# Kernel tuning notes

Measured on AMD Instinct MI355X. Metric: run time of the kernel, lower is better.

Reference implementation:

```python
import jax, jax.numpy as jnp
import numpy as np

B, IN, OUT, P, NS = 256, 1024, 512, 1000, 128

def setup_inputs() -> dict:
    key = jax.random.key(0)
    ks = jax.random.split(key, 6)
    return {
        "x": jax.random.normal(ks[0], (B, IN), jnp.float32),
        "noise": jax.random.normal(ks[1], (B, NS, P), jnp.float32),
        "fb_w": jax.random.normal(ks[2], (1, IN), jnp.float32) * (1.0 / np.sqrt(IN)),
        "fb_b": jnp.zeros((1,), jnp.float32),
        "decay_param": jnp.full((1,), 0.1, jnp.float32),
        "conv_w": jax.random.normal(ks[3], (P, P, 3), jnp.float32) * (1.0 / np.sqrt(3 * P)),
        "conv_b": jnp.zeros((P,), jnp.float32),
        "out_w": jax.random.normal(ks[4], (OUT, P), jnp.float32) * (1.0 / np.sqrt(P)),
        "out_b": jnp.zeros((OUT,), jnp.float32),
    }


def reference(x, noise, fb_w, fb_b, decay_param, conv_w, conv_b, out_w, out_b):
    # x: [B, IN]; noise: [B, NS, P] (Brownian increments for the SDE kernel)
    n_steps = noise.shape[1]
    dt = 1.0 / n_steps                       # T = 1.0
    sd = jnp.sqrt(jnp.asarray(dt, x.dtype))
    # per-sample feedback value: sigmoid(feedback_controller(x))
    feedback = jax.nn.sigmoid(x @ fb_w.T + fb_b)            # [B, 1]
    # decay value: sigmoid(decay_controller) * 0.5 (scalar)
    decay = jax.nn.sigmoid(decay_param[0]) * 0.5
    retain = 1.0 - decay * dt
    # Batched Euler-Maruyama Brownian SDE: X_{t+1} = (1 - decay*dt) X_t + feedback*sqrt(dt)*eps_t
    eps = jnp.transpose(noise, (1, 0, 2))                    # [NS, B, P]
    x0 = jnp.zeros((x.shape[0], noise.shape[2]), x.dtype)

    def step(X, e):
        Xn = X * retain + feedback * sd * e
        return Xn, Xn

    _, paths = jax.lax.scan(step, x0, eps)                   # [NS, B, P]
    paths_bct = jnp.transpose(paths, (1, 2, 0))              # [B, P, NS]
    # temporal_aggregator: Conv1d(P, P, kernel=3, padding=1) over time, then mean over time
    agg = jax.lax.conv_general_dilated(
        paths_bct, conv_w, window_strides=(1,), padding=[(1, 1)],
        dimension_numbers=("NCH", "OIH", "NCH"))
    agg = (agg + conv_b[None, :, None]).mean(axis=2)         # [B, P]
    # output_projection: P -> OUT
    return agg @ out_w.T + out_b
```

## Files before the change

### kernel.cpp

```cpp
#include <hip/hip_runtime.h>
#include <hip/hip_bf16.h>

#define B_N   256
#define IN_N  1024
#define OUT_N 512
#define P_N   1000
#define NS_N  128

#define K1P   3072
#define N1P   1024
#define K2P   1024
#define SK1   16
#define SK2   8

typedef __attribute__((ext_vector_type(8))) short short8v;
typedef __attribute__((ext_vector_type(4))) float f32x4;
typedef unsigned short ushort_t;

__device__ __forceinline__ float sigmoid_f(float z) { return 1.0f / (1.0f + __expf(-z)); }

__device__ __forceinline__ ushort_t f2bf(float x) {
    return __bfloat16_as_ushort(__float2bfloat16(x));
}

__global__ __launch_bounds__(256) void sde_fused_kernel(const float* __restrict__ x,
                                                        const float* __restrict__ fb_w,
                                                        const float* __restrict__ fb_b,
                                                        const float* __restrict__ noise,
                                                        const float* __restrict__ decay_param,
                                                        ushort_t* __restrict__ Thi) {
    const int b  = blockIdx.x;
    const int ch = blockIdx.y;
    const int t  = threadIdx.x;
    const int cg = t & 127;
    const int th = t >> 7;

    float4 xv = ((const float4*)(x + (size_t)b * IN_N))[t];
    float4 wv = ((const float4*)fb_w)[t];
    float s = xv.x * wv.x + xv.y * wv.y + xv.z * wv.z + xv.w * wv.w;
    __shared__ float red[256];
    red[t] = s;
    __syncthreads();
    for (int off = 128; off >= 1; off >>= 1) {
        if (t < off) red[t] += red[t + off];
        __syncthreads();
    }
    float fbv = sigmoid_f(red[0] + fb_b[0]);

    float decay = sigmoid_f(decay_param[0]) * 0.5f;
    const float dt = 1.0f / NS_N;
    float retain = 1.0f - decay * dt;
    float inv_omr = 1.0f / (decay * dt);
    float r2 = retain * retain, r4 = r2 * r2, r8 = r4 * r4;
    float r16 = r8 * r8, r32 = r16 * r16, r64 = r32 * r32;

    const int c0 = ch * 512 + cg * 4;
    const bool act = (c0 < P_N);

    float4 sE = {0, 0, 0, 0}, L = {0, 0, 0, 0}, F = {0, 0, 0, 0};
    if (act) {
        const float* base = noise + (size_t)b * NS_N * P_N + c0;
        const int s0 = th * 64;
        float rp = 1.0f;
        #pragma unroll 16
        for (int ss = s0 + 63; ss >= s0; --ss) {
            float4 e = *(const float4*)(base + (size_t)ss * P_N);
            sE.x += e.x; sE.y += e.y; sE.z += e.z; sE.w += e.w;
            L.x += rp * e.x; L.y += rp * e.y; L.z += rp * e.z; L.w += rp * e.w;
            if (ss == 0) F = e;
            rp *= retain;
        }
    }

    __shared__ float4 xSE[128], xL[128], xF[128];
    if (th == 0) { xSE[cg] = sE; xL[cg] = L; xF[cg] = F; }
    __syncthreads();

    if (th == 1) {
        size_t tb = (size_t)b * K1P + 3 * (size_t)c0;
        if (!act) {
            #pragma unroll
            for (int j = 0; j < 12; ++j) Thi[tb + j] = 0;
            return;
        }
        float4 se0 = xSE[cg], ll0 = xL[cg], ff = xF[cg];
        float Se[4] = {se0.x + sE.x, se0.y + sE.y, se0.z + sE.z, se0.w + sE.w};
        float Lv[4] = {L.x + r64 * ll0.x, L.y + r64 * ll0.y, L.z + r64 * ll0.z, L.w + r64 * ll0.w};
        float Fv[4] = {ff.x, ff.y, ff.z, ff.w};
        float sd = sqrtf(dt);
        float scale = fbv * sd * (1.0f / NS_N);
        #pragma unroll
        for (int j = 0; j < 4; ++j) {
            float Aj = (Se[j] - retain * Lv[j]) * inv_omr;
            Thi[tb + 3 * j + 0] = f2bf(scale * (Aj - Lv[j]));
            Thi[tb + 3 * j + 1] = f2bf(scale * Aj);
            Thi[tb + 3 * j + 2] = f2bf(scale * (Aj - Fv[j]));
        }
    }
}

__global__ __launch_bounds__(512) void gemm_bf16_mfma(const ushort_t* __restrict__ A,
                                                      const float* __restrict__ B,
                                                      float* __restrict__ Cpart,
                                                      int lda, int ldb,
                                                      int Nvalid, int Kvalid,
                                                      int Kper, int ldc) {
    __shared__ __align__(16) ushort_t As[128 * 64];
    __shared__ __align__(16) ushort_t Bs[128 * 64];

    const int tid  = threadIdx.x;
    const int lane = tid & 63;
    const int wave = tid >> 6;
    const int r15  = lane & 15;
    const int g4   = lane >> 4;
    const int wrow = wave >> 2;
    const int wcol = wave & 3;
    const int n0 = blockIdx.x * 128;
    const int m0 = blockIdx.y * 128;
    const size_t kbeg = (size_t)blockIdx.z * Kper;

    f32x4 acc[4][2] = {};

    for (int kt = 0; kt < Kper; kt += 64) {
        const size_t kk0 = kbeg + kt;
        #pragma unroll
        for (int c = 0; c < 2; ++c) {
            int chunk = tid + c * 512;
            int row = chunk >> 3;
            int g   = chunk & 7;
            int ldsoff = row * 64 + ((g ^ (row & 7)) << 3);

            const size_t ka = (size_t)(m0 + row) * lda + kk0 + g * 8;
            *(short8v*)&As[ldsoff] = *(const short8v*)(A + ka);

            short8v bh = {0, 0, 0, 0, 0, 0, 0, 0};
            if ((n0 + row) < Nvalid && (int)(kk0 + g * 8) < Kvalid) {
                const float* bp = B + (size_t)(n0 + row) * ldb + kk0 + g * 8;
                float4 b0 = *(const float4*)bp;
                float4 b1 = *(const float4*)(bp + 4);
                bh[0] = (short)f2bf(b0.x); bh[1] = (short)f2bf(b0.y);
                bh[2] = (short)f2bf(b0.z); bh[3] = (short)f2bf(b0.w);
                bh[4] = (short)f2bf(b1.x); bh[5] = (short)f2bf(b1.y);
                bh[6] = (short)f2bf(b1.z); bh[7] = (short)f2bf(b1.w);
            }
            *(short8v*)&Bs[ldsoff] = bh;
        }
        __syncthreads();

        #pragma unroll
        for (int ks = 0; ks < 2; ++ks) {
            const int g = ks * 4 + g4;
            short8v af[4], bf_[2];
            #pragma unroll
            for (int f = 0; f < 4; ++f) {
                int arow = wrow * 64 + f * 16 + r15;
                af[f] = *(const short8v*)&As[arow * 64 + ((g ^ (arow & 7)) << 3)];
            }
            #pragma unroll
            for (int f = 0; f < 2; ++f) {
                int brow = wcol * 32 + f * 16 + r15;
                bf_[f] = *(const short8v*)&Bs[brow * 64 + ((g ^ (brow & 7)) << 3)];
            }
            #pragma unroll
            for (int mf = 0; mf < 4; ++mf) {
                #pragma unroll
                for (int nf = 0; nf < 2; ++nf) {
                    acc[mf][nf] = __builtin_amdgcn_mfma_f32_16x16x32_bf16(af[mf], bf_[nf], acc[mf][nf], 0, 0, 0);
                }
            }
        }
        __syncthreads();
    }

    float* cp = Cpart + (size_t)blockIdx.z * B_N * ldc;
    #pragma unroll
    for (int mf = 0; mf < 4; ++mf) {
        #pragma unroll
        for (int nf = 0; nf < 2; ++nf) {
            #pragma unroll
            for (int r = 0; r < 4; ++r) {
                int m = m0 + wrow * 64 + mf * 16 + g4 * 4 + r;
                int n = n0 + wcol * 32 + nf * 16 + r15;
                cp[(size_t)m * ldc + n] = acc[mf][nf][r];
            }
        }
    }
}

__global__ __launch_bounds__(256) void reduce_agg_kernel(const float* __restrict__ Cpart1,
                                                         const float* __restrict__ conv_b,
                                                         ushort_t* __restrict__ agg) {
    int idx = blockIdx.x * 256 + threadIdx.x;
    int n = idx & (N1P - 1);
    float s = 0.f;
    if (n < P_N) {
        s = conv_b[n];
        #pragma unroll
        for (int z = 0; z < SK1; ++z) s += Cpart1[(size_t)z * (B_N * N1P) + idx];
    }
    agg[idx] = f2bf(s);
}

__global__ __launch_bounds__(256) void reduce_out_kernel(const float* __restrict__ Cpart2,
                                                         const float* __restrict__ out_b,
                                                         float* __restrict__ out) {
    int idx = blockIdx.x * 256 + threadIdx.x;
    int n = idx & (OUT_N - 1);
    float s = out_b[n];
    #pragma unroll
    for (int z = 0; z < SK2; ++z) s += Cpart2[(size_t)z * (B_N * OUT_N) + idx];
    out[idx] = s;
}

extern "C" void kernel_launch(void* const* d_in, const int* in_sizes, int n_in,
                              void* d_out, int out_size, void* d_ws, size_t ws_size,
                              hipStream_t stream) {
    const float* x           = (const float*)d_in[0];
    const float* noise       = (const float*)d_in[1];
    const float* fb_w        = (const float*)d_in[2];
    const float* fb_b        = (const float*)d_in[3];
    const float* decay_param = (const float*)d_in[4];
    const float* conv_w      = (const float*)d_in[5];
    const float* conv_b      = (const float*)d_in[6];
    const float* out_w       = (const float*)d_in[7];
    const float* out_b       = (const float*)d_in[8];
    float* out = (float*)d_out;

    char* ws = (char*)d_ws;
    size_t off = 0;
    ushort_t* Thi    = (ushort_t*)(ws + off); off += (size_t)B_N * K1P * 2;
    ushort_t* agg    = (ushort_t*)(ws + off); off += (size_t)B_N * K2P * 2;
    float*    Cpart1 = (float*)(ws + off);    off += (size_t)SK1 * B_N * N1P * 4;
    float*    Cpart2 = (float*)(ws + off);    off += (size_t)SK2 * B_N * OUT_N * 4;

    {
        dim3 grid(B_N, 2);
        sde_fused_kernel<<<grid, 256, 0, stream>>>(x, fb_w, fb_b, noise, decay_param, Thi);
    }

    {
        dim3 grid(N1P / 128, B_N / 128, SK1);
        gemm_bf16_mfma<<<grid, 512, 0, stream>>>(Thi, conv_w, Cpart1,
                                                 K1P, 3 * P_N, P_N, 3 * P_N,
                                                 K1P / SK1, N1P);
    }

    reduce_agg_kernel<<<(B_N * N1P) / 256, 256, 0, stream>>>(Cpart1, conv_b, agg);

    {
        dim3 grid(OUT_N / 128, B_N / 128, SK2);
        gemm_bf16_mfma<<<grid, 512, 0, stream>>>(agg, out_w, Cpart2,
                                                 K2P, P_N, OUT_N, P_N,
                                                 K2P / SK2, OUT_N);
    }

    reduce_out_kernel<<<(B_N * OUT_N) / 256, 256, 0, stream>>>(Cpart2, out_b, out);
}
```

Measured before the change: 52.60 us.

## Use full-M GEMM tiles, bf16 split-K partials, vectorized reductions, 4-way SDE time split

The GEMM now covers the whole batch (M=256) per block with a 4x4 MFMA fragment tile per wave. This halves the grid and reads each conv_w/out_w tile only once. Split-K partials are stored as bf16 instead of fp32, halving partial-sum traffic, and the reduction kernels read and write four elements per thread. The SDE kernel splits the time dimension across four thread groups of 512 threads for more memory parallelism. The trade-offs are fewer GEMM blocks, which lowers occupancy and CU coverage, and extra rounding error from bf16 partials.

```diff
diff --git a/kernel.cpp b/kernel.cpp
--- a/kernel.cpp
+++ b/kernel.cpp
@@ -16,14 +16,19 @@
 typedef __attribute__((ext_vector_type(8))) short short8v;
 typedef __attribute__((ext_vector_type(4))) float f32x4;
 typedef unsigned short ushort_t;
+typedef __attribute__((ext_vector_type(4))) unsigned short ushort4v;
 
 __device__ __forceinline__ float sigmoid_f(float z) { return 1.0f / (1.0f + __expf(-z)); }
 
 __device__ __forceinline__ ushort_t f2bf(float x) {
     return __bfloat16_as_ushort(__float2bfloat16(x));
 }
-
-__global__ __launch_bounds__(256) void sde_fused_kernel(const float* __restrict__ x,
+__device__ __forceinline__ float bf2f(ushort_t h) {
+    union { unsigned u; float f; } v; v.u = ((unsigned)h) << 16;
+    return v.f;
+}
+
+__global__ __launch_bounds__(512) void sde_fused_kernel(const float* __restrict__ x,
                                                         const float* __restrict__ fb_w,
                                                         const float* __restrict__ fb_b,
                                                         const float* __restrict__ noise,
@@ -33,15 +38,14 @@
     const int ch = blockIdx.y;
     const int t  = threadIdx.x;
     const int cg = t & 127;
-    const int th = t >> 7;
-
-    float4 xv = ((const float4*)(x + (size_t)b * IN_N))[t];
-    float4 wv = ((const float4*)fb_w)[t];
-    float s = xv.x * wv.x + xv.y * wv.y + xv.z * wv.z + xv.w * wv.w;
-    __shared__ float red[256];
-    red[t] = s;
+    const int tq = t >> 7;
+
+    float2 xv = ((const float2*)(x + (size_t)b * IN_N))[t];
+    float2 wv = ((const float2*)fb_w)[t];
+    __shared__ float red[512];
+    red[t] = xv.x * wv.x + xv.y * wv.y;
     __syncthreads();
-    for (int off = 128; off >= 1; off >>= 1) {
+    for (int off = 256; off >= 1; off >>= 1) {
         if (t < off) red[t] += red[t + off];
         __syncthreads();
     }
@@ -52,40 +56,46 @@
     float retain = 1.0f - decay * dt;
     float inv_omr = 1.0f / (decay * dt);
     float r2 = retain * retain, r4 = r2 * r2, r8 = r4 * r4;
-    float r16 = r8 * r8, r32 = r16 * r16, r64 = r32 * r32;
+    float r16 = r8 * r8, r32 = r16 * r16;
+    float r64 = r32 * r32, r96 = r64 * r32;
 
     const int c0 = ch * 512 + cg * 4;
     const bool act = (c0 < P_N);
-
-    float4 sE = {0, 0, 0, 0}, L = {0, 0, 0, 0}, F = {0, 0, 0, 0};
+    const float* base = noise + (size_t)b * NS_N * P_N + (act ? c0 : 0);
+
+    float4 sE = {0, 0, 0, 0}, L = {0, 0, 0, 0};
     if (act) {
-        const float* base = noise + (size_t)b * NS_N * P_N + c0;
-        const int s0 = th * 64;
+        const int s0 = tq * 32;
         float rp = 1.0f;
-        #pragma unroll 16
-        for (int ss = s0 + 63; ss >= s0; --ss) {
+        #pragma unroll 8
+        for (int ss = s0 + 31; ss >= s0; --ss) {
             float4 e = *(const float4*)(base + (size_t)ss * P_N);
             sE.x += e.x; sE.y += e.y; sE.z += e.z; sE.w += e.w;
             L.x += rp * e.x; L.y += rp * e.y; L.z += rp * e.z; L.w += rp * e.w;
-            if (ss == 0) F = e;
             rp *= retain;
         }
     }
 
-    __shared__ float4 xSE[128], xL[128], xF[128];
-    if (th == 0) { xSE[cg] = sE; xL[cg] = L; xF[cg] = F; }
+    __shared__ float4 xSE[3][128], xL[3][128], xF[128];
+    if (tq < 3) { xSE[tq][cg] = sE; xL[tq][cg] = L; }
+    if (tq == 0 && act) xF[cg] = *(const float4*)base;
     __syncthreads();
 
-    if (th == 1) {
+    if (tq == 3) {
         size_t tb = (size_t)b * K1P + 3 * (size_t)c0;
         if (!act) {
             #pragma unroll
             for (int j = 0; j < 12; ++j) Thi[tb + j] = 0;
             return;
         }
-        float4 se0 = xSE[cg], ll0 = xL[cg], ff = xF[cg];
-        float Se[4] = {se0.x + sE.x, se0.y + sE.y, se0.z + sE.z, se0.w + sE.w};
-        float Lv[4] = {L.x + r64 * ll0.x, L.y + r64 * ll0.y, L.z + r64 * ll0.z, L.w + r64 * ll0.w};
+        float4 se0 = xSE[0][cg], se1 = xSE[1][cg], se2 = xSE[2][cg];
+        float4 l0 = xL[0][cg], l1 = xL[1][cg], l2 = xL[2][cg], ff = xF[cg];
+        float Se[4] = {se0.x + se1.x + se2.x + sE.x, se0.y + se1.y + se2.y + sE.y,
+                       se0.z + se1.z + se2.z + sE.z, se0.w + se1.w + se2.w + sE.w};
+        float Lv[4] = {L.x + r32 * l2.x + r64 * l1.x + r96 * l0.x,
+                       L.y + r32 * l2.y + r64 * l1.y + r96 * l0.y,
+                       L.z + r32 * l2.z + r64 * l1.z + r96 * l0.z,
+                       L.w + r32 * l2.w + r64 * l1.w + r96 * l0.w};
         float Fv[4] = {ff.x, ff.y, ff.z, ff.w};
         float sd = sqrtf(dt);
         float scale = fbv * sd * (1.0f / NS_N);
@@ -99,13 +109,13 @@
     }
 }
 
-__global__ __launch_bounds__(512) void gemm_bf16_mfma(const ushort_t* __restrict__ A,
-                                                      const float* __restrict__ B,
-                                                      float* __restrict__ Cpart,
-                                                      int lda, int ldb,
-                                                      int Nvalid, int Kvalid,
-                                                      int Kper, int ldc) {
-    __shared__ __align__(16) ushort_t As[128 * 64];
+__global__ __launch_bounds__(512) void gemm_bf16_bm256(const ushort_t* __restrict__ A,
+                                                       const float* __restrict__ B,
+                                                       ushort_t* __restrict__ Cpart,
+                                                       int lda, int ldb,
+                                                       int Nvalid, int Kvalid,
+                                                       int Kper, int ldc) {
+    __shared__ __align__(16) ushort_t As[256 * 64];
     __shared__ __align__(16) ushort_t Bs[128 * 64];
 
     const int tid  = threadIdx.x;
@@ -113,29 +123,33 @@
     const int wave = tid >> 6;
     const int r15  = lane & 15;
     const int g4   = lane >> 4;
-    const int wrow = wave >> 2;
-    const int wcol = wave & 3;
+    const int wrow = wave >> 1;
+    const int wcol = wave & 1;
     const int n0 = blockIdx.x * 128;
-    const int m0 = blockIdx.y * 128;
     const size_t kbeg = (size_t)blockIdx.z * Kper;
 
-    f32x4 acc[4][2] = {};
+    f32x4 acc[4][4] = {};
 
     for (int kt = 0; kt < Kper; kt += 64) {
         const size_t kk0 = kbeg + kt;
+        #pragma unroll
+        for (int c = 0; c < 4; ++c) {
+            int chunk = tid + c * 512;
+            int row = chunk >> 3;
+            int g   = chunk & 7;
+            int ldsoff = row * 64 + ((g ^ (row & 7)) << 3);
+            *(short8v*)&As[ldsoff] = *(const short8v*)(A + (size_t)row * lda + kk0 + g * 8);
+        }
         #pragma unroll
         for (int c = 0; c < 2; ++c) {
             int chunk = tid + c * 512;
             int row = chunk >> 3;
             int g   = chunk & 7;
             int ldsoff = row * 64 + ((g ^ (row & 7)) << 3);
-
-            const size_t ka = (size_t)(m0 + row) * lda + kk0 + g * 8;
-            *(short8v*)&As[ldsoff] = *(const short8v*)(A + ka);
-
+            int k = (int)kk0 + g * 8;
             short8v bh = {0, 0, 0, 0, 0, 0, 0, 0};
-            if ((n0 + row) < Nvalid && (int)(kk0 + g * 8) < Kvalid) {
-                const float* bp = B + (size_t)(n0 + row) * ldb + kk0 + g * 8;
+            if ((n0 + row) < Nvalid && k < Kvalid) {
+                const float* bp = B + (size_t)(n0 + row) * ldb + k;
                 float4 b0 = *(const float4*)bp;
                 float4 b1 = *(const float4*)(bp + 4);
                 bh[0] = (short)f2bf(b0.x); bh[1] = (short)f2bf(b0.y);
@@ -150,21 +164,21 @@
         #pragma unroll
         for (int ks = 0; ks < 2; ++ks) {
             const int g = ks * 4 + g4;
-            short8v af[4], bf_[2];
+            short8v af[4], bf_[4];
             #pragma unroll
             for (int f = 0; f < 4; ++f) {
                 int arow = wrow * 64 + f * 16 + r15;
                 af[f] = *(const short8v*)&As[arow * 64 + ((g ^ (arow & 7)) << 3)];
             }
             #pragma unroll
-            for (int f = 0; f < 2; ++f) {
-                int brow = wcol * 32 + f * 16 + r15;
+            for (int f = 0; f < 4; ++f) {
+                int brow = wcol * 64 + f * 16 + r15;
                 bf_[f] = *(const short8v*)&Bs[brow * 64 + ((g ^ (brow & 7)) << 3)];
             }
             #pragma unroll
             for (int mf = 0; mf < 4; ++mf) {
                 #pragma unroll
-                for (int nf = 0; nf < 2; ++nf) {
+                for (int nf = 0; nf < 4; ++nf) {
                     acc[mf][nf] = __builtin_amdgcn_mfma_f32_16x16x32_bf16(af[mf], bf_[nf], acc[mf][nf], 0, 0, 0);
                 }
             }
@@ -172,44 +186,54 @@
         __syncthreads();
     }
 
-    float* cp = Cpart + (size_t)blockIdx.z * B_N * ldc;
+    ushort_t* cp = Cpart + (size_t)blockIdx.z * B_N * ldc;
     #pragma unroll
     for (int mf = 0; mf < 4; ++mf) {
         #pragma unroll
-        for (int nf = 0; nf < 2; ++nf) {
+        for (int nf = 0; nf < 4; ++nf) {
             #pragma unroll
             for (int r = 0; r < 4; ++r) {
-                int m = m0 + wrow * 64 + mf * 16 + g4 * 4 + r;
-                int n = n0 + wcol * 32 + nf * 16 + r15;
-                cp[(size_t)m * ldc + n] = acc[mf][nf][r];
-            }
-        }
-    }
-}
-
-__global__ __launch_bounds__(256) void reduce_agg_kernel(const float* __restrict__ Cpart1,
+                int m = wrow * 64 + mf * 16 + g4 * 4 + r;
+                int n = n0 + wcol * 64 + nf * 16 + r15;
+                cp[(size_t)m * ldc + n] = f2bf(acc[mf][nf][r]);
+            }
+        }
+    }
+}
+
+__global__ __launch_bounds__(256) void reduce_agg_kernel(const ushort_t* __restrict__ Cpart1,
                                                          const float* __restrict__ conv_b,
                                                          ushort_t* __restrict__ agg) {
-    int idx = blockIdx.x * 256 + threadIdx.x;
-    int n = idx & (N1P - 1);
-    float s = 0.f;
+    int idx4 = (blockIdx.x * 256 + threadIdx.x) * 4;
+    int n = idx4 & (N1P - 1);
+    float s0 = 0.f, s1 = 0.f, s2 = 0.f, s3 = 0.f;
     if (n < P_N) {
-        s = conv_b[n];
-        #pragma unroll
-        for (int z = 0; z < SK1; ++z) s += Cpart1[(size_t)z * (B_N * N1P) + idx];
-    }
-    agg[idx] = f2bf(s);
-}
-
-__global__ __launch_bounds__(256) void reduce_out_kernel(const float* __restrict__ Cpart2,
+        float4 cb = *(const float4*)(conv_b + n);
+        s0 = cb.x; s1 = cb.y; s2 = cb.z; s3 = cb.w;
+        #pragma unroll
+        for (int z = 0; z < SK1; ++z) {
+            ushort4v p = *(const ushort4v*)(Cpart1 + (size_t)z * (B_N * N1P) + idx4);
+            s0 += bf2f(p[0]); s1 += bf2f(p[1]); s2 += bf2f(p[2]); s3 += bf2f(p[3]);
+        }
+    }
+    ushort4v o = {f2bf(s0), f2bf(s1), f2bf(s2), f2bf(s3)};
+    *(ushort4v*)(agg + idx4) = o;
+}
+
+__global__ __launch_bounds__(256) void reduce_out_kernel(const ushort_t* __restrict__ Cpart2,
                                                          const float* __restrict__ out_b,
                                                          float* __restrict__ out) {
-    int idx = blockIdx.x * 256 + threadIdx.x;
-    int n = idx & (OUT_N - 1);
-    float s = out_b[n];
+    int idx4 = (blockIdx.x * 256 + threadIdx.x) * 4;
+    int n = idx4 & (OUT_N - 1);
+    float4 ob = *(const float4*)(out_b + n);
+    float s0 = ob.x, s1 = ob.y, s2 = ob.z, s3 = ob.w;
     #pragma unroll
-    for (int z = 0; z < SK2; ++z) s += Cpart2[(size_t)z * (B_N * OUT_N) + idx];
-    out[idx] = s;
+    for (int z = 0; z < SK2; ++z) {
+        ushort4v p = *(const ushort4v*)(Cpart2 + (size_t)z * (B_N * OUT_N) + idx4);
+        s0 += bf2f(p[0]); s1 += bf2f(p[1]); s2 += bf2f(p[2]); s3 += bf2f(p[3]);
+    }
+    float4 o = {s0, s1, s2, s3};
+    *(float4*)(out + idx4) = o;
 }
 
 extern "C" void kernel_launch(void* const* d_in, const int* in_sizes, int n_in,
@@ -230,29 +254,29 @@
     size_t off = 0;
     ushort_t* Thi    = (ushort_t*)(ws + off); off += (size_t)B_N * K1P * 2;
     ushort_t* agg    = (ushort_t*)(ws + off); off += (size_t)B_N * K2P * 2;
-    float*    Cpart1 = (float*)(ws + off);    off += (size_t)SK1 * B_N * N1P * 4;
-    float*    Cpart2 = (float*)(ws + off);    off += (size_t)SK2 * B_N * OUT_N * 4;
+    ushort_t* Cpart1 = (ushort_t*)(ws + off); off += (size_t)SK1 * B_N * N1P * 2;
+    ushort_t* Cpart2 = (ushort_t*)(ws + off); off += (size_t)SK2 * B_N * OUT_N * 2;
 
     {
         dim3 grid(B_N, 2);
-        sde_fused_kernel<<<grid, 256, 0, stream>>>(x, fb_w, fb_b, noise, decay_param, Thi);
+        sde_fused_kernel<<<grid, 512, 0, stream>>>(x, fb_w, fb_b, noise, decay_param, Thi);
     }
 
     {
-        dim3 grid(N1P / 128, B_N / 128, SK1);
-        gemm_bf16_mfma<<<grid, 512, 0, stream>>>(Thi, conv_w, Cpart1,
-                                                 K1P, 3 * P_N, P_N, 3 * P_N,
-                                                 K1P / SK1, N1P);
-    }
-
-    reduce_agg_kernel<<<(B_N * N1P) / 256, 256, 0, stream>>>(Cpart1, conv_b, agg);
+        dim3 grid(N1P / 128, 1, SK1);
+        gemm_bf16_bm256<<<grid, 512, 0, stream>>>(Thi, conv_w, Cpart1,
+                                                  K1P, 3 * P_N, P_N, 3 * P_N,
+                                                  K1P / SK1, N1P);
+    }
+
+    reduce_agg_kernel<<<(B_N * N1P) / 1024, 256, 0, stream>>>(Cpart1, conv_b, agg);
 
     {
-        dim3 grid(OUT_N / 128, B_N / 128, SK2);
-        gemm_bf16_mfma<<<grid, 512, 0, stream>>>(agg, out_w, Cpart2,
-                                                 K2P, P_N, OUT_N, P_N,
-                                                 K2P / SK2, OUT_N);
-    }
-
-    reduce_out_kernel<<<(B_N * OUT_N) / 256, 256, 0, stream>>>(Cpart2, out_b, out);
-}
+        dim3 grid(OUT_N / 128, 1, SK2);
+        gemm_bf16_bm256<<<grid, 512, 0, stream>>>(agg, out_w, Cpart2,
+                                                  K2P, P_N, OUT_N, P_N,
+                                                  K2P / SK2, OUT_N);
+    }
+
+    reduce_out_kernel<<<(B_N * OUT_N) / 1024, 256, 0, stream>>>(Cpart2, out_b, out);
+}
```

Result: faster. 48.39 us (-8.0%).
